# Kernel tuning notes

Measured on AMD Instinct MI355X. Metric: run time of the kernel, lower is better.

The kernel has to match this reference:

```python
import jax, jax.numpy as jnp
import numpy as np

N = 8192       # nodes == in_channels (diff matrix is NxN)
DF = 256       # feature dim of z
E = 65536      # edges (unused by forward, kept for signature fidelity)
M = 4096       # len(reliable_negatives)
NEG = 10       # neg_samples
STEPS = 10     # num_diffusion_steps
TEMP = 0.2


def setup_inputs() -> dict:
    key = jax.random.key(0)
    k1, k2, k3, k4, k5 = jax.random.split(key, 5)
    z = jax.random.normal(k1, (N, DF), dtype=jnp.float32)
    # learned parameter; init positive-uniform so row sums are well conditioned
    diff_matrix = jax.random.uniform(k2, (N, N), dtype=jnp.float32)
    edge_index = jax.random.randint(k3, (2, E), 0, N)
    reliable_negatives = jax.random.randint(k4, (M,), 0, N)
    # deterministic stand-in for torch.randint(0, len(reliable_negatives), (neg_samples,))
    neg_idx = jax.random.randint(k5, (NEG,), 0, M)
    return {"z": z, "diff_matrix": diff_matrix, "edge_index": edge_index,
            "reliable_negatives": reliable_negatives, "neg_idx": neg_idx}


def _l2norm(x):
    # F.normalize(dim=1): divide by L2 norm clamped at 1e-12
    n = jnp.sqrt(jnp.sum(x * x, axis=1, keepdims=True))
    return x / jnp.maximum(n, 1e-12)


def reference(z, diff_matrix, edge_index, reliable_negatives, neg_idx):
    # 10-step loop: mm(inverse(diag(rowsum)), M) == row-wise reciprocal scaling
    dm = diff_matrix
    for _ in range(STEPS):
        dm = dm / jnp.sum(dm, axis=1, keepdims=True)  # [N, N]
    # (normalized_diff_matrix with +eps*I is computed in the original but unused)

    anchor = z                       # [N, DF]
    positive = dm @ z                # [N, DF] diffused features
    negative = z[neg_idx]            # [NEG, DF]

    a = _l2norm(anchor)
    p = _l2norm(positive)
    n = _l2norm(negative)

    pos_sim = jnp.sum(a * p, axis=1) / TEMP                 # [N]
    neg_sim = jnp.exp(jnp.einsum('nd,kd->nk', a, n) / TEMP)  # [N, NEG]
    loss = -jnp.log(jnp.exp(pos_sim) / (jnp.exp(pos_sim) + neg_sim.sum(axis=1))).mean()
    return loss
```

## Files before the change

### kernel.cpp

```cpp
#include <hip/hip_runtime.h>
#include <hip/hip_bf16.h>


typedef float f32x4 __attribute__((ext_vector_type(4)));
typedef short s16x8 __attribute__((ext_vector_type(8)));

#define NN 8192
#define DFF 256
#define NNEG 10

__device__ __forceinline__ unsigned short f2bf(float x) {
  return __builtin_bit_cast(unsigned short, __float2bfloat16(x));
}

__device__ __forceinline__ void gload_lds16(const void* g, void* l) {
  __builtin_amdgcn_global_load_lds(
      (const __attribute__((address_space(1))) void*)(void*)g,
      (__attribute__((address_space(3))) void*)l, 16, 0, 0);
}

__device__ __forceinline__ float dot4(float4 a, float4 b) {
  return a.x * b.x + a.y * b.y + a.z * b.z + a.w * b.w;
}

__global__ void k_transpose(const float* __restrict__ z,
                            unsigned short* __restrict__ zT) {
  __shared__ float tile[64][65];
  const int bx = blockIdx.x;
  const int by = blockIdx.y;
  const int t = threadIdx.x;
  const int lc = t & 63, lq = t >> 6;
#pragma unroll
  for (int p = 0; p < 16; ++p) {
    const int lr = lq * 16 + p;
    tile[lr][lc] = z[(size_t)(bx * 64 + lr) * DFF + by * 64 + lc];
  }
  __syncthreads();
#pragma unroll
  for (int p = 0; p < 16; ++p) {
    const int tc = lq * 16 + p;
    zT[(size_t)(by * 64 + tc) * NN + bx * 64 + lc] = f2bf(tile[lc][tc]);
  }
}

__global__ void k_neg(const float* __restrict__ z, const int* __restrict__ neg_idx,
                      float* __restrict__ negn) {
  const int l = threadIdx.x;
#pragma unroll
  for (int k = 0; k < NNEG; ++k) {
    const int idx = neg_idx[k];
    float4 v = *(const float4*)(z + (size_t)idx * DFF + l * 4);
    float ss = dot4(v, v);
#pragma unroll
    for (int off = 32; off > 0; off >>= 1) ss += __shfl_xor(ss, off);
    const float s = 1.0f / fmaxf(sqrtf(ss), 1e-12f);
    float4 o;
    o.x = v.x * s; o.y = v.y * s; o.z = v.z * s; o.w = v.w * s;
    *(float4*)(negn + k * DFF + l * 4) = o;
  }
}

__global__ __launch_bounds__(256, 2) void k_gemm(const float* __restrict__ dm,
                                                 const unsigned short* __restrict__ zT,
                                                 float* __restrict__ part, int KS) {
  __shared__ unsigned short sA[64 * 64];
  __shared__ unsigned short sB[256 * 64];
  const int bx = blockIdx.x;
  const int mtile = bx & 127;
  const int ks = bx >> 7;
  const int klen = NN / KS;
  const int k0 = ks * klen;
  const int steps = klen / 64;
  const int tid = threadIdx.x;
  const int w = tid >> 6;
  const int l = tid & 63;
  const int m0 = mtile * 64;

  f32x4 acc[4][4] = {};

  const int ar = tid >> 4;
  const int ac = (tid & 15) * 4;

  const int rq = l >> 3;
  const int bsw = (l & 7) * 16;
  const int blog = bsw ^ (rq << 4);

  for (int kt = 0; kt < steps; ++kt) {
    const int kb = k0 + kt * 64;
#pragma unroll
    for (int p = 0; p < 4; ++p) {
      const int r = p * 16 + ar;
      const float4 v = *(const float4*)(dm + (size_t)(m0 + r) * NN + kb + ac);
      ushort4 h;
      h.x = f2bf(v.x); h.y = f2bf(v.y); h.z = f2bf(v.z); h.w = f2bf(v.w);
      *(ushort4*)&sA[r * 64 + (ac ^ ((r & 7) << 3))] = h;
    }
    {
      const char* srcbase = (const char*)zT + (size_t)kb * 2 + blog;
#pragma unroll
      for (int q = 0; q < 8; ++q) {
        const int rn = w * 64 + q * 8 + rq;
        gload_lds16(srcbase + (size_t)rn * (NN * 2),
                    (char*)sB + (w * 64 + q * 8) * 128);
      }
    }
    __syncthreads();
#pragma unroll
    for (int kc = 0; kc < 2; ++kc) {
      const int e = kc * 32 + (l >> 4) * 8;
      s16x8 af[4], bfr[4];
#pragma unroll
      for (int mi = 0; mi < 4; ++mi) {
        const int r = mi * 16 + (l & 15);
        af[mi] = *(const s16x8*)&sA[r * 64 + (e ^ ((r & 7) << 3))];
      }
#pragma unroll
      for (int nj = 0; nj < 4; ++nj) {
        const int rn = w * 64 + nj * 16 + (l & 15);
        bfr[nj] = *(const s16x8*)&sB[rn * 64 + (e ^ ((rn & 7) << 3))];
      }
#pragma unroll
      for (int mi = 0; mi < 4; ++mi)
#pragma unroll
        for (int nj = 0; nj < 4; ++nj)
          acc[mi][nj] = __builtin_amdgcn_mfma_f32_16x16x32_bf16(
              af[mi], bfr[nj], acc[mi][nj], 0, 0, 0);
    }
    __syncthreads();
  }
  float* cb = part + (size_t)ks * NN * DFF;
#pragma unroll
  for (int mi = 0; mi < 4; ++mi)
#pragma unroll
    for (int nj = 0; nj < 4; ++nj) {
      const int col = w * 64 + nj * 16 + (l & 15);
      const int row0 = m0 + mi * 16 + (l >> 4) * 4;
#pragma unroll
      for (int r = 0; r < 4; ++r)
        cb[(size_t)(row0 + r) * DFF + col] = acc[mi][nj][r];
    }
}

__global__ __launch_bounds__(256) void k_loss(const float* __restrict__ z,
                                              const float* __restrict__ part,
                                              const float* __restrict__ negn,
                                              float* __restrict__ lpart, int KS) {
  __shared__ float sneg[NNEG * DFF];
  __shared__ float swsum[4];
  const int t = threadIdx.x;
  for (int j = t; j < NNEG * DFF; j += 256) sneg[j] = negn[j];
  __syncthreads();
  const int w = t >> 6, l = t & 63;
  const int gw = blockIdx.x * 4 + w;
  float lsum = 0.f;
  for (int rr = 0; rr < 8; ++rr) {
    const int i = gw * 8 + rr;
    const float4 a = *(const float4*)(z + (size_t)i * DFF + l * 4);
    float4 p; p.x = 0.f; p.y = 0.f; p.z = 0.f; p.w = 0.f;
    for (int ksp = 0; ksp < KS; ++ksp) {
      const float4 q = *(const float4*)(part + ((size_t)ksp * NN + i) * DFF + l * 4);
      p.x += q.x; p.y += q.y; p.z += q.z; p.w += q.w;
    }
    float vals[13];
    vals[0] = dot4(a, a);
    vals[1] = dot4(p, p);
    vals[2] = dot4(a, p);
#pragma unroll
    for (int k = 0; k < NNEG; ++k) {
      const float4 nv = *(const float4*)&sneg[k * DFF + l * 4];
      vals[3 + k] = dot4(a, nv);
    }
#pragma unroll
    for (int off = 32; off > 0; off >>= 1)
#pragma unroll
      for (int j = 0; j < 13; ++j) vals[j] += __shfl_xor(vals[j], off);
    const float na = fmaxf(sqrtf(vals[0]), 1e-12f);
    const float npp = fmaxf(sqrtf(vals[1]), 1e-12f);
    const float ps = vals[2] / (na * npp) * 5.0f;
    float S = 0.f;
#pragma unroll
    for (int k = 0; k < NNEG; ++k) S += expf(vals[3 + k] / na * 5.0f);
    lsum += logf(expf(ps) + S) - ps;
  }
  if (l == 0) swsum[w] = lsum;
  __syncthreads();
  if (t == 0) lpart[blockIdx.x] = swsum[0] + swsum[1] + swsum[2] + swsum[3];
}

__global__ void k_final(const float* __restrict__ lpart, float* __restrict__ out) {
  const int t = threadIdx.x;
  float v = lpart[t] + lpart[t + 64] + lpart[t + 128] + lpart[t + 192];
#pragma unroll
  for (int off = 32; off > 0; off >>= 1) v += __shfl_xor(v, off);
  if (t == 0) out[0] = v * (1.0f / (float)NN);
}

extern "C" void kernel_launch(void* const* d_in, const int* in_sizes, int n_in,
                              void* d_out, int out_size, void* d_ws, size_t ws_size,
                              hipStream_t stream) {
  const float* z = (const float*)d_in[0];
  const float* dm = (const float*)d_in[1];
  const int* neg_idx = (const int*)d_in[4];
  float* out = (float*)d_out;

  auto need = [](size_t ks) {
    return (size_t)4 * 1024 * 1024 + ks * (size_t)NN * DFF * 4 + 10240 + 1024;
  };
  int KS = 4;
  if (ws_size < need(4)) KS = (ws_size >= need(2)) ? 2 : 1;

  char* ws = (char*)d_ws;
  unsigned short* zT = (unsigned short*)ws;
  float* part = (float*)(ws + (size_t)4 * 1024 * 1024);
  float* negn = (float*)(ws + (size_t)4 * 1024 * 1024 + (size_t)KS * NN * DFF * 4);
  float* lpart = (float*)((char*)negn + NNEG * DFF * 4);

  k_transpose<<<dim3(128, 4), 256, 0, stream>>>(z, zT);
  k_neg<<<1, 64, 0, stream>>>(z, neg_idx, negn);
  k_gemm<<<128 * KS, 256, 0, stream>>>(dm, zT, part, KS);
  k_loss<<<256, 256, 0, stream>>>(z, part, negn, lpart, KS);
  k_final<<<1, 64, 0, stream>>>(lpart, out);
}
```

Measured before the change: 128.8 us.

## Double-buffer GEMM LDS tiles and fold negative normalization into loss kernel

The GEMM now uses two LDS buffers: while MFMAs run on the current tile, it prefetches the next A tile from fp32 global memory into registers and issues async global-to-LDS loads for the next B tile, then writes A to the other buffer after compute. This hides global load latency behind matrix math and leaves one barrier per iteration. Separately, the tiny k_neg kernel is removed and each k_loss block normalizes the negatives itself, saving one launch. LDS use doubles (about 80KB per block), which may limit occupancy against the requested 2 blocks per CU. Every loss block also repeats the negative normalization.

```diff
diff --git a/kernel.cpp b/kernel.cpp
--- a/kernel.cpp
+++ b/kernel.cpp
@@ -43,28 +43,11 @@
   }
 }
 
-__global__ void k_neg(const float* __restrict__ z, const int* __restrict__ neg_idx,
-                      float* __restrict__ negn) {
-  const int l = threadIdx.x;
-#pragma unroll
-  for (int k = 0; k < NNEG; ++k) {
-    const int idx = neg_idx[k];
-    float4 v = *(const float4*)(z + (size_t)idx * DFF + l * 4);
-    float ss = dot4(v, v);
-#pragma unroll
-    for (int off = 32; off > 0; off >>= 1) ss += __shfl_xor(ss, off);
-    const float s = 1.0f / fmaxf(sqrtf(ss), 1e-12f);
-    float4 o;
-    o.x = v.x * s; o.y = v.y * s; o.z = v.z * s; o.w = v.w * s;
-    *(float4*)(negn + k * DFF + l * 4) = o;
-  }
-}
-
 __global__ __launch_bounds__(256, 2) void k_gemm(const float* __restrict__ dm,
                                                  const unsigned short* __restrict__ zT,
                                                  float* __restrict__ part, int KS) {
-  __shared__ unsigned short sA[64 * 64];
-  __shared__ unsigned short sB[256 * 64];
+  __shared__ unsigned short sA[2][64 * 64];
+  __shared__ unsigned short sB[2][256 * 64];
   const int bx = blockIdx.x;
   const int mtile = bx & 127;
   const int ks = bx >> 7;
@@ -85,26 +68,41 @@
   const int bsw = (l & 7) * 16;
   const int blog = bsw ^ (rq << 4);
 
+  float4 areg[4];
+
+#define LOAD_A(kt)                                                             \
+  _Pragma("unroll") for (int p = 0; p < 4; ++p) areg[p] =                      \
+      *(const float4*)(dm + (size_t)(m0 + p * 16 + ar) * NN + k0 + (kt)*64 + ac);
+
+#define WRITE_A(buf)                                                           \
+  _Pragma("unroll") for (int p = 0; p < 4; ++p) {                              \
+    const int r = p * 16 + ar;                                                 \
+    ushort4 h;                                                                 \
+    h.x = f2bf(areg[p].x); h.y = f2bf(areg[p].y);                              \
+    h.z = f2bf(areg[p].z); h.w = f2bf(areg[p].w);                              \
+    *(ushort4*)&sA[buf][r * 64 + (ac ^ ((r & 7) << 3))] = h;                   \
+  }
+
+#define STAGE_B(kt, buf)                                                       \
+  {                                                                            \
+    const char* srcbase = (const char*)zT + (size_t)(k0 + (kt)*64) * 2 + blog; \
+    _Pragma("unroll") for (int q = 0; q < 8; ++q) {                            \
+      gload_lds16(srcbase + (size_t)(w * 64 + q * 8 + rq) * (NN * 2),          \
+                  (char*)sB[buf] + (w * 64 + q * 8) * 128);                    \
+    }                                                                          \
+  }
+
+  STAGE_B(0, 0);
+  LOAD_A(0);
+  WRITE_A(0);
+  __syncthreads();
+
   for (int kt = 0; kt < steps; ++kt) {
-    const int kb = k0 + kt * 64;
-#pragma unroll
-    for (int p = 0; p < 4; ++p) {
-      const int r = p * 16 + ar;
-      const float4 v = *(const float4*)(dm + (size_t)(m0 + r) * NN + kb + ac);
-      ushort4 h;
-      h.x = f2bf(v.x); h.y = f2bf(v.y); h.z = f2bf(v.z); h.w = f2bf(v.w);
-      *(ushort4*)&sA[r * 64 + (ac ^ ((r & 7) << 3))] = h;
-    }
-    {
-      const char* srcbase = (const char*)zT + (size_t)kb * 2 + blog;
-#pragma unroll
-      for (int q = 0; q < 8; ++q) {
-        const int rn = w * 64 + q * 8 + rq;
-        gload_lds16(srcbase + (size_t)rn * (NN * 2),
-                    (char*)sB + (w * 64 + q * 8) * 128);
-      }
-    }
-    __syncthreads();
+    const int cur = kt & 1, nxt = cur ^ 1;
+    if (kt + 1 < steps) {
+      LOAD_A(kt + 1);
+      STAGE_B(kt + 1, nxt);
+    }
 #pragma unroll
     for (int kc = 0; kc < 2; ++kc) {
       const int e = kc * 32 + (l >> 4) * 8;
@@ -112,12 +110,12 @@
 #pragma unroll
       for (int mi = 0; mi < 4; ++mi) {
         const int r = mi * 16 + (l & 15);
-        af[mi] = *(const s16x8*)&sA[r * 64 + (e ^ ((r & 7) << 3))];
+        af[mi] = *(const s16x8*)&sA[cur][r * 64 + (e ^ ((r & 7) << 3))];
       }
 #pragma unroll
       for (int nj = 0; nj < 4; ++nj) {
         const int rn = w * 64 + nj * 16 + (l & 15);
-        bfr[nj] = *(const s16x8*)&sB[rn * 64 + (e ^ ((rn & 7) << 3))];
+        bfr[nj] = *(const s16x8*)&sB[cur][rn * 64 + (e ^ ((rn & 7) << 3))];
       }
 #pragma unroll
       for (int mi = 0; mi < 4; ++mi)
@@ -126,8 +124,12 @@
           acc[mi][nj] = __builtin_amdgcn_mfma_f32_16x16x32_bf16(
               af[mi], bfr[nj], acc[mi][nj], 0, 0, 0);
     }
+    if (kt + 1 < steps) {
+      WRITE_A(nxt);
+    }
     __syncthreads();
   }
+
   float* cb = part + (size_t)ks * NN * DFF;
 #pragma unroll
   for (int mi = 0; mi < 4; ++mi)
@@ -139,18 +141,31 @@
       for (int r = 0; r < 4; ++r)
         cb[(size_t)(row0 + r) * DFF + col] = acc[mi][nj][r];
     }
+#undef LOAD_A
+#undef WRITE_A
+#undef STAGE_B
 }
 
 __global__ __launch_bounds__(256) void k_loss(const float* __restrict__ z,
                                               const float* __restrict__ part,
-                                              const float* __restrict__ negn,
+                                              const int* __restrict__ neg_idx,
                                               float* __restrict__ lpart, int KS) {
   __shared__ float sneg[NNEG * DFF];
   __shared__ float swsum[4];
   const int t = threadIdx.x;
-  for (int j = t; j < NNEG * DFF; j += 256) sneg[j] = negn[j];
-  __syncthreads();
   const int w = t >> 6, l = t & 63;
+  for (int k = w; k < NNEG; k += 4) {
+    const int idx = neg_idx[k];
+    float4 v = *(const float4*)(z + (size_t)idx * DFF + l * 4);
+    float ss = dot4(v, v);
+#pragma unroll
+    for (int off = 32; off > 0; off >>= 1) ss += __shfl_xor(ss, off);
+    const float s = 1.0f / fmaxf(sqrtf(ss), 1e-12f);
+    float4 o;
+    o.x = v.x * s; o.y = v.y * s; o.z = v.z * s; o.w = v.w * s;
+    *(float4*)&sneg[k * DFF + l * 4] = o;
+  }
+  __syncthreads();
   const int gw = blockIdx.x * 4 + w;
   float lsum = 0.f;
   for (int rr = 0; rr < 8; ++rr) {
@@ -204,7 +219,7 @@
   float* out = (float*)d_out;
 
   auto need = [](size_t ks) {
-    return (size_t)4 * 1024 * 1024 + ks * (size_t)NN * DFF * 4 + 10240 + 1024;
+    return (size_t)4 * 1024 * 1024 + ks * (size_t)NN * DFF * 4 + 1024;
   };
   int KS = 4;
   if (ws_size < need(4)) KS = (ws_size >= need(2)) ? 2 : 1;
@@ -212,12 +227,10 @@
   char* ws = (char*)d_ws;
   unsigned short* zT = (unsigned short*)ws;
   float* part = (float*)(ws + (size_t)4 * 1024 * 1024);
-  float* negn = (float*)(ws + (size_t)4 * 1024 * 1024 + (size_t)KS * NN * DFF * 4);
-  float* lpart = (float*)((char*)negn + NNEG * DFF * 4);
+  float* lpart = (float*)(ws + (size_t)4 * 1024 * 1024 + (size_t)KS * NN * DFF * 4);
 
   k_transpose<<<dim3(128, 4), 256, 0, stream>>>(z, zT);
-  k_neg<<<1, 64, 0, stream>>>(z, neg_idx, negn);
   k_gemm<<<128 * KS, 256, 0, stream>>>(dm, zT, part, KS);
-  k_loss<<<256, 256, 0, stream>>>(z, part, negn, lpart, KS);
+  k_loss<<<256, 256, 0, stream>>>(z, part, neg_idx, lpart, KS);
   k_final<<<1, 64, 0, stream>>>(lpart, out);
 }
```

Result: faster. 124.7 us (-3.2%).
